# Kernel tuning notes

Hardware: AMD Instinct MI355X
Metric: run time of the kernel (lower is better)

Reference implementation:

```python
import jax, jax.numpy as jnp
import numpy as np

N_NODES = 100000
N_EDGES = 600000
D = 128


def setup_inputs() -> dict:
    key = jax.random.key(0)
    ks = jax.random.split(key, 12)
    inp = {
        'feat': jax.random.normal(ks[0], (N_NODES, D), dtype=jnp.float32),
        'W_tran': jax.random.normal(ks[1], (D, D), dtype=jnp.float32) * (1.0 / np.sqrt(D)),
        'att_w1': jax.random.normal(ks[2], (4 * D, D), dtype=jnp.float32) * (1.0 / np.sqrt(D)),
        'att_b1': jax.random.normal(ks[3], (4 * D,), dtype=jnp.float32) * 0.01,
        'att_w2': jax.random.normal(ks[4], (1, 4 * D), dtype=jnp.float32) * (1.0 / np.sqrt(4 * D)),
        'trans_w': jax.random.uniform(ks[5], (N_EDGES,), dtype=jnp.float32),
        'geo_src': jax.random.randint(ks[6], (N_EDGES,), 0, N_NODES, dtype=jnp.int32),
        'geo_dst': jax.random.randint(ks[7], (N_EDGES,), 0, N_NODES, dtype=jnp.int32),
        'cat_src': jax.random.randint(ks[8], (N_EDGES,), 0, N_NODES, dtype=jnp.int32),
        'cat_dst': jax.random.randint(ks[9], (N_EDGES,), 0, N_NODES, dtype=jnp.int32),
        'trans_src': jax.random.randint(ks[10], (N_EDGES,), 0, N_NODES, dtype=jnp.int32),
        'trans_dst': jax.random.randint(ks[11], (N_EDGES,), 0, N_NODES, dtype=jnp.int32),
    }
    return inp


def _mean_agg(f, src, dst, n):
    # copy_u('f','m') then mean('m', .) : gather src feats, segment-mean by dst
    msum = jax.ops.segment_sum(f[src], dst, num_segments=n)
    cnt = jax.ops.segment_sum(jnp.ones((src.shape[0],), f.dtype), dst, num_segments=n)
    return msum / jnp.maximum(cnt, 1.0)[:, None]


def reference(feat, W_tran, att_w1, att_b1, att_w2, trans_w,
              geo_src, geo_dst, cat_src, cat_dst, trans_src, trans_dst):
    n = feat.shape[0]
    # feat_tran: Linear(D, D, bias=False) -> x @ W^T
    f = feat @ W_tran.T
    geo = _mean_agg(f, geo_src, geo_dst, n)            # [N, D]
    cat = _mean_agg(f, cat_src, cat_dst, n)            # [N, D]
    # u_mul_e('f','w') then sum: weighted gather + segment-sum by dst
    trans = jax.ops.segment_sum(f[trans_src] * trans_w[:, None], trans_dst, num_segments=n)
    z = jnp.stack([geo, trans, cat], axis=1)           # [N, 3, D]
    # SemanticAttention: Linear -> tanh -> Linear(no bias), mean over nodes, softmax over relations
    h = jnp.tanh(jnp.einsum('nrd,hd->nrh', z, att_w1) + att_b1)   # [N, 3, 4D]
    w = jnp.einsum('nrh,oh->nro', h, att_w2).mean(0)              # [3, 1]
    beta = jax.nn.softmax(w, axis=0)                              # [3, 1]
    fused = (beta[None, :, :] * z).sum(1)                         # [N, D]
    return jax.nn.leaky_relu(fused, negative_slope=0.2)
```

## Files before the change

kernel.cpp:

```cpp
#include <hip/hip_runtime.h>
#include <math.h>

#define DD 128
#define NNODES 100000
#define NEDGES 600000
#define NREL 3
#define MTOT (NREL*NNODES)
#define NTILES (NNODES/16)
#define RT_PER_BLK 8
#define NBLK_REL ((NTILES + RT_PER_BLK - 1)/RT_PER_BLK)
#define ATT_WAVES 8

#define BSHIFT 10
#define NBUCK ((NNODES + 1023) >> BSHIFT)
#define GBUCK (NREL*NBUCK)
#define CAP 8192
#define P1_THREADS 512
#define P1_EPT 8
#define P1_EPB (P1_THREADS*P1_EPT)
#define P1_BLOCKS ((NREL*NEDGES + P1_EPB - 1)/P1_EPB)

typedef __attribute__((ext_vector_type(8))) short short8;
typedef __attribute__((ext_vector_type(4))) float f32x4;

__device__ inline float bf2f(unsigned short u){ return __uint_as_float(((unsigned int)u)<<16); }
__device__ inline float bflo(unsigned int u){ return __uint_as_float(u<<16); }
__device__ inline float bfhi(unsigned int u){ return __uint_as_float(u & 0xffff0000u); }
__device__ inline unsigned short f2bf(float f){
    unsigned int i = __float_as_uint(f);
    unsigned int r = (i + 0x7fffu + ((i>>16)&1u)) >> 16;
    return (unsigned short)r;
}
__device__ inline unsigned int pack2(float lo, float hi){
    return (unsigned int)f2bf(lo) | ((unsigned int)f2bf(hi) << 16);
}
__device__ inline short8 cvt8(const float* __restrict__ p){
    f32x4 a = *(const f32x4*)p;
    f32x4 b = *(const f32x4*)(p+4);
    short8 t;
    t[0]=(short)f2bf(a[0]); t[1]=(short)f2bf(a[1]); t[2]=(short)f2bf(a[2]); t[3]=(short)f2bf(a[3]);
    t[4]=(short)f2bf(b[0]); t[5]=(short)f2bf(b[1]); t[6]=(short)f2bf(b[2]); t[7]=(short)f2bf(b[3]);
    return t;
}

__global__ __launch_bounds__(256) void k_cvt2(
    const float* __restrict__ ina, unsigned short* __restrict__ outa, int na4,
    const float* __restrict__ inb, unsigned short* __restrict__ outb, int nb4)
{
    int gid = blockIdx.x*256 + threadIdx.x;
    const float* in; unsigned short* out; int idx;
    if (gid < na4){ in = ina; out = outa; idx = gid; }
    else { idx = gid - na4; if (idx >= nb4) return; in = inb; out = outb; }
    f32x4 v = ((const f32x4*)in)[idx];
    ushort4 o;
    o.x=f2bf(v[0]); o.y=f2bf(v[1]); o.z=f2bf(v[2]); o.w=f2bf(v[3]);
    ((ushort4*)out)[idx] = o;
}

__global__ __launch_bounds__(256) void k_transform(
    const float* __restrict__ feat, const unsigned short* __restrict__ Wbf,
    unsigned short* __restrict__ f_out)
{
    int wid = blockIdx.x*4 + (threadIdx.x>>6);
    if (wid >= NNODES/16) return;
    int lane = threadIdx.x & 63;
    int m = lane & 15, quad = lane >> 4;
    int n0 = wid*16;

    short8 a[4];
    const float* arow = feat + (size_t)(n0+m)*DD;
    #pragma unroll
    for (int ks=0; ks<4; ++ks) a[ks] = cvt8(arow + ks*32 + quad*8);

    #pragma unroll
    for (int ct=0; ct<8; ++ct){
        f32x4 acc = {0.f,0.f,0.f,0.f};
        const short8* brow = (const short8*)(Wbf + (size_t)(ct*16+m)*DD);
        #pragma unroll
        for (int ks=0; ks<4; ++ks){
            acc = __builtin_amdgcn_mfma_f32_16x16x32_bf16(a[ks], brow[ks*4+quad], acc, 0,0,0);
        }
        int col = ct*16 + m;
        #pragma unroll
        for (int i=0;i<4;++i)
            f_out[(size_t)(n0+quad*4+i)*DD + col] = f2bf(acc[i]);
    }
}

__global__ __launch_bounds__(P1_THREADS) void k_part(
    const int* __restrict__ s0, const int* __restrict__ d0,
    const int* __restrict__ s1, const int* __restrict__ d1,
    const int* __restrict__ s2, const int* __restrict__ d2,
    const float* __restrict__ tw,
    int* __restrict__ bcur,
    int2* __restrict__ slab, float* __restrict__ wslab)
{
    __shared__ int hist[GBUCK];
    for (int i=threadIdx.x; i<GBUCK; i+=P1_THREADS) hist[i]=0;
    __syncthreads();

    int e0 = blockIdx.x * P1_EPB;
    int ss[P1_EPT], dd_[P1_EPT], gb[P1_EPT]; float wv[P1_EPT];
    #pragma unroll
    for (int j=0;j<P1_EPT;++j){
        int e = e0 + j*P1_THREADS + threadIdx.x;
        gb[j] = -1;
        if (e < NREL*NEDGES){
            int rel = e / NEDGES; int i = e - rel*NEDGES;
            const int* s = (rel==0)?s0:(rel==1)?s1:s2;
            const int* d = (rel==0)?d0:(rel==1)?d1:d2;
            ss[j]=s[i]; dd_[j]=d[i];
            wv[j] = (rel==2)? tw[i] : 0.f;
            gb[j] = rel*NBUCK + (dd_[j]>>BSHIFT);
            atomicAdd(&hist[gb[j]], 1);
        }
    }
    __syncthreads();
    for (int i=threadIdx.x; i<GBUCK; i+=P1_THREADS){
        int c = hist[i];
        hist[i] = (c>0) ? atomicAdd(&bcur[i], c) : 0;
    }
    __syncthreads();
    #pragma unroll
    for (int j=0;j<P1_EPT;++j){
        if (gb[j] >= 0){
            int off = atomicAdd(&hist[gb[j]], 1);
            int2 pr; pr.x = ss[j]; pr.y = dd_[j];
            slab[(size_t)gb[j]*CAP + off] = pr;
            if (gb[j] >= 2*NBUCK) wslab[(size_t)(gb[j]-2*NBUCK)*CAP + off] = wv[j];
        }
    }
}

__global__ __launch_bounds__(512) void k_bscan(const int* __restrict__ bcur,
                                               int* __restrict__ bbase)
{
    __shared__ int sm[512];
    int t = threadIdx.x;
    sm[t] = (t<GBUCK)? bcur[t] : 0; __syncthreads();
    for (int off=1; off<512; off<<=1){
        int x = (t>=off)? sm[t-off] : 0;
        __syncthreads(); sm[t]+=x; __syncthreads();
    }
    if (t<GBUCK) bbase[t] = (t>0)? sm[t-1] : 0;
}

__global__ __launch_bounds__(512) void k_csr(
    const int2* __restrict__ slab, const float* __restrict__ wslab,
    const int* __restrict__ bcur, const int* __restrict__ bbase,
    int* __restrict__ offs, int* __restrict__ cnt,
    int* __restrict__ es, float* __restrict__ ewt)
{
    __shared__ int lcnt[1024];
    __shared__ int lsc[1024];
    __shared__ int psum[512];
    int gb = blockIdx.x;
    int rel = gb / NBUCK, b = gb - rel*NBUCK;
    int n0 = b << BSHIFT;
    int nn = min(1024, NNODES - n0);
    int ecount = bcur[gb];
    int base = bbase[gb];
    const int2* ep = slab + (size_t)gb*CAP;
    int t = threadIdx.x;

    lcnt[2*t] = 0; lcnt[2*t+1] = 0;
    __syncthreads();
    for (int i=t; i<ecount; i+=512)
        atomicAdd(&lcnt[ep[i].y - n0], 1);
    __syncthreads();
    int v0 = lcnt[2*t], v1 = lcnt[2*t+1];
    psum[t] = v0 + v1; __syncthreads();
    for (int off=1; off<512; off<<=1){
        int x = (t>=off)? psum[t-off] : 0;
        __syncthreads(); psum[t]+=x; __syncthreads();
    }
    int ex = (t>0)? psum[t-1] : 0;
    lsc[2*t] = ex; lsc[2*t+1] = ex + v0;
    __syncthreads();
    int relN = rel*NNODES;
    for (int i=t; i<nn; i+=512){
        offs[relN + n0 + i] = base + lsc[i];
        cnt [relN + n0 + i] = lcnt[i];
    }
    __syncthreads();
    for (int i=t; i<ecount; i+=512){
        int2 pr = ep[i];
        int pos = base + atomicAdd(&lsc[pr.y - n0], 1);
        es[pos] = pr.x;
        if (rel==2) ewt[pos - 2*NEDGES] = wslab[(size_t)b*CAP + i];
    }
}

__global__ __launch_bounds__(256) void k_agg(
    const unsigned short* __restrict__ f,
    const int* __restrict__ es, const float* __restrict__ ewt,
    const int* __restrict__ offs, const int* __restrict__ cnt,
    unsigned short* __restrict__ z)
{
    int gid = blockIdx.x*256 + threadIdx.x;
    int g = gid >> 4;
    if (g >= MTOT) return;
    int c = gid & 15;
    int rel = g / NNODES;
    int start = offs[g];
    int deg   = cnt[g];

    float a0=0,a1=0,a2=0,a3=0,a4=0,a5=0,a6=0,a7=0;
    int i = 0;
    for (; i+1 < deg; i += 2){
        int s0 = es[start+i], s1 = es[start+i+1];
        uint4 v0 = *(const uint4*)(f + (size_t)s0*DD + c*8);
        uint4 v1 = *(const uint4*)(f + (size_t)s1*DD + c*8);
        float w0 = (rel==2) ? ewt[start+i   - 2*NEDGES] : 1.f;
        float w1 = (rel==2) ? ewt[start+i+1 - 2*NEDGES] : 1.f;
        a0 += w0*bflo(v0.x); a1 += w0*bfhi(v0.x);
        a2 += w0*bflo(v0.y); a3 += w0*bfhi(v0.y);
        a4 += w0*bflo(v0.z); a5 += w0*bfhi(v0.z);
        a6 += w0*bflo(v0.w); a7 += w0*bfhi(v0.w);
        a0 += w1*bflo(v1.x); a1 += w1*bfhi(v1.x);
        a2 += w1*bflo(v1.y); a3 += w1*bfhi(v1.y);
        a4 += w1*bflo(v1.z); a5 += w1*bfhi(v1.z);
        a6 += w1*bflo(v1.w); a7 += w1*bfhi(v1.w);
    }
    if (i < deg){
        int s = es[start+i];
        float w = (rel==2) ? ewt[start+i - 2*NEDGES] : 1.f;
        uint4 v = *(const uint4*)(f + (size_t)s*DD + c*8);
        a0 += w*bflo(v.x); a1 += w*bfhi(v.x);
        a2 += w*bflo(v.y); a3 += w*bfhi(v.y);
        a4 += w*bflo(v.z); a5 += w*bfhi(v.z);
        a6 += w*bflo(v.w); a7 += w*bfhi(v.w);
    }
    float sc = (rel<2) ? 1.f/fmaxf((float)deg, 1.f) : 1.f;
    uint4 o;
    o.x = pack2(a0*sc, a1*sc);
    o.y = pack2(a2*sc, a3*sc);
    o.z = pack2(a4*sc, a5*sc);
    o.w = pack2(a6*sc, a7*sc);
    *(uint4*)(z + (size_t)g*DD + c*8) = o;
}

__global__ __launch_bounds__(512, 4) void k_att(
    const unsigned short* __restrict__ z,
    const unsigned short* __restrict__ w1,
    const float* __restrict__ bias1,
    const float* __restrict__ wv2,
    float* __restrict__ w_part)
{
    __shared__ uint4 sm[RT_PER_BLK*256];
    __shared__ float sred[ATT_WAVES];
    const float C2 = 2.8853900817779268f;

    int rel = blockIdx.x / NBLK_REL;
    int nb  = blockIdx.x % NBLK_REL;
    int trt0 = nb * RT_PER_BLK;
    int rt_count = min(RT_PER_BLK, NTILES - trt0);
    int row0 = trt0 * 16;
    const unsigned short* zrel = z + (size_t)rel*NNODES*DD;

    int lane = threadIdx.x & 63;
    int wv   = threadIdx.x >> 6;
    int m = lane & 15, quad = lane >> 4;

    short8 bq[16];
    float ww[4], bbc[4];
    #pragma unroll
    for (int ct=0; ct<4; ++ct){
        int col = (wv*4 + ct)*16 + m;
        const short8* brow = (const short8*)(w1 + (size_t)col*DD);
        #pragma unroll
        for (int ks=0; ks<4; ++ks) bq[ct*4+ks] = brow[ks*4 + quad];
        ww[ct]  = wv2[col];
        bbc[ct] = bias1[col] * C2;
    }

    int valid_rows = rt_count * 16;
    #pragma unroll
    for (int i=0; i<4; ++i){
        int u = i*512 + threadIdx.x;
        int row = u >> 4, kc = u & 15;
        if (row < valid_rows){
            uint4 v = *(const uint4*)(zrel + (size_t)(row0+row)*DD + kc*8);
            int rt = row >> 4, mm = row & 15;
            sm[rt*256 + kc*16 + (mm ^ kc)] = v;
        }
    }
    __syncthreads();

    const short8* smx = (const short8*)sm;
    float s_r[4] = {0.f,0.f,0.f,0.f};
    for (int rt=0; rt<rt_count; ++rt){
        int base = rt*256;
        short8 a0 = smx[base + (0  + quad)*16 + (m ^ (0  + quad))];
        short8 a1 = smx[base + (4  + quad)*16 + (m ^ (4  + quad))];
        short8 a2 = smx[base + (8  + quad)*16 + (m ^ (8  + quad))];
        short8 a3 = smx[base + (12 + quad)*16 + (m ^ (12 + quad))];
        #pragma unroll
        for (int ct=0; ct<4; ++ct){
            f32x4 acc = {0.f,0.f,0.f,0.f};
            acc = __builtin_amdgcn_mfma_f32_16x16x32_bf16(a0, bq[ct*4+0], acc, 0,0,0);
            acc = __builtin_amdgcn_mfma_f32_16x16x32_bf16(a1, bq[ct*4+1], acc, 0,0,0);
            acc = __builtin_amdgcn_mfma_f32_16x16x32_bf16(a2, bq[ct*4+2], acc, 0,0,0);
            acc = __builtin_amdgcn_mfma_f32_16x16x32_bf16(a3, bq[ct*4+3], acc, 0,0,0);
            #pragma unroll
            for (int i=0;i<4;++i){
                float e = __builtin_amdgcn_exp2f(__builtin_fmaf(acc[i], C2, bbc[ct]));
                s_r[ct] += __builtin_amdgcn_rcpf(e + 1.f);
            }
        }
    }
    float s_all = 0.f;
    #pragma unroll
    for (int ct=0; ct<4; ++ct)
        s_all += ww[ct]*(float)(4*rt_count) - 2.f*ww[ct]*s_r[ct];
    #pragma unroll
    for (int off=32; off; off>>=1) s_all += __shfl_xor(s_all, off);
    if (lane == 0) sred[wv] = s_all;
    __syncthreads();
    if (threadIdx.x == 0){
        float tt = 0.f;
        #pragma unroll
        for (int i=0;i<ATT_WAVES;++i) tt += sred[i];
        atomicAdd(&w_part[rel], tt);
    }
}

__global__ __launch_bounds__(256) void k_final(
    const unsigned short* __restrict__ z0, const unsigned short* __restrict__ z1,
    const unsigned short* __restrict__ z2,
    const float* __restrict__ w_part, float* __restrict__ out)
{
    int gid = blockIdx.x*256 + threadIdx.x;
    if (gid >= NNODES*DD/4) return;
    const float invN = 1.f / (float)NNODES;
    float w0 = w_part[0]*invN, w1 = w_part[1]*invN, w2 = w_part[2]*invN;
    float mx = fmaxf(w0, fmaxf(w1, w2));
    const float LOG2E = 1.4426950408889634f;
    float e0 = __builtin_amdgcn_exp2f((w0-mx)*LOG2E);
    float e1 = __builtin_amdgcn_exp2f((w1-mx)*LOG2E);
    float e2 = __builtin_amdgcn_exp2f((w2-mx)*LOG2E);
    float inv = 1.f/(e0+e1+e2);
    float b0 = e0*inv, b1 = e1*inv, b2 = e2*inv;
    ushort4 g = ((const ushort4*)z0)[gid];
    ushort4 t = ((const ushort4*)z1)[gid];
    ushort4 c = ((const ushort4*)z2)[gid];
    f32x4 o;
    float gv[4] = {bf2f(g.x),bf2f(g.y),bf2f(g.z),bf2f(g.w)};
    float tv[4] = {bf2f(t.x),bf2f(t.y),bf2f(t.z),bf2f(t.w)};
    float cv[4] = {bf2f(c.x),bf2f(c.y),bf2f(c.z),bf2f(c.w)};
    #pragma unroll
    for (int i=0;i<4;++i){
        float x = b0*gv[i] + b1*tv[i] + b2*cv[i];
        o[i] = (x > 0.f) ? x : 0.2f*x;
    }
    ((f32x4*)out)[gid] = o;
}

extern "C" void kernel_launch(void* const* d_in, const int* in_sizes, int n_in,
                              void* d_out, int out_size, void* d_ws, size_t ws_size,
                              hipStream_t stream)
{
    const float* feat = (const float*)d_in[0];
    const float* W    = (const float*)d_in[1];
    const float* aw1  = (const float*)d_in[2];
    const float* ab1  = (const float*)d_in[3];
    const float* aw2  = (const float*)d_in[4];
    const float* tw   = (const float*)d_in[5];
    const int* geo_src   = (const int*)d_in[6];
    const int* geo_dst   = (const int*)d_in[7];
    const int* cat_src   = (const int*)d_in[8];
    const int* cat_dst   = (const int*)d_in[9];
    const int* trans_src = (const int*)d_in[10];
    const int* trans_dst = (const int*)d_in[11];

    char* ws = (char*)d_ws;
    float* w_part = (float*)ws;
    int*   bcur   = (int*)(w_part + 64);
    int*   bbase  = bcur + 320;
    int*   offs   = bbase + 320;
    int*   cnt    = offs + MTOT;
    unsigned short* w1_bf = (unsigned short*)(cnt + MTOT);
    unsigned short* w_bf  = w1_bf + 512*DD;
    int*   es     = (int*)(w_bf + DD*DD);
    float* ewt    = (float*)(es + NREL*NEDGES);
    unsigned short* z = (unsigned short*)(ewt + NEDGES);
    int2*  slab   = (int2*)z;
    float* wslab  = (float*)(slab + (size_t)GBUCK*CAP);
    unsigned short* f_bf = (unsigned short*)d_out;

    (void)hipMemsetAsync(w_part, 0, (64 + 320)*sizeof(int), stream);

    int na4 = 512*DD/4, nb4 = DD*DD/4;
    k_cvt2<<<(na4 + nb4 + 255)/256, 256, 0, stream>>>(aw1, w1_bf, na4, W, w_bf, nb4);
    k_transform<<<(NNODES/16 + 3)/4, 256, 0, stream>>>(feat, w_bf, f_bf);

    k_part<<<P1_BLOCKS, P1_THREADS, 0, stream>>>(geo_src, geo_dst, cat_src, cat_dst,
                                                 trans_src, trans_dst, tw,
                                                 bcur, slab, wslab);
    k_bscan<<<1, 512, 0, stream>>>(bcur, bbase);
    k_csr<<<GBUCK, 512, 0, stream>>>(slab, wslab, bcur, bbase, offs, cnt, es, ewt);

    k_agg<<<(MTOT*16 + 255)/256, 256, 0, stream>>>(f_bf, es, ewt, offs, cnt, z);

    k_att<<<NREL*NBLK_REL, 512, 0, stream>>>(z, w1_bf, ab1, aw2, w_part);

    unsigned short* z_geo   = z;
    unsigned short* z_cat   = z + (size_t)NNODES*DD;
    unsigned short* z_trans = z + (size_t)2*NNODES*DD;
    int dg = (NNODES*DD/4 + 255)/256;
    k_final<<<dg, 256, 0, stream>>>(z_geo, z_cat, z_trans, w_part, (float*)d_out);
}
```

Measured before the change: 356.4 us.

## Fuse neighbor aggregation into attention kernel, writing tiles straight to LDS

Merges the separate aggregation kernel into the attention-score kernel. Each block aggregates its own 128 rows per relation and writes each result both to global z (still needed by the final kernel) and directly into the swizzled shared-memory tile. This removes one launch and the re-read of z from global memory before the MFMA stage. The trade-off is that the gather now runs under the attention kernel's launch bounds and occupancy. Each thread also handles four rows in sequence, which may limit latency hiding for the irregular gathers.

```diff
diff --git a/kernel.cpp b/kernel.cpp
--- a/kernel.cpp
+++ b/kernel.cpp
@@ -191,60 +191,14 @@
     }
 }
 
-__global__ __launch_bounds__(256) void k_agg(
+__global__ __launch_bounds__(512, 4) void k_aggatt(
     const unsigned short* __restrict__ f,
     const int* __restrict__ es, const float* __restrict__ ewt,
     const int* __restrict__ offs, const int* __restrict__ cnt,
-    unsigned short* __restrict__ z)
-{
-    int gid = blockIdx.x*256 + threadIdx.x;
-    int g = gid >> 4;
-    if (g >= MTOT) return;
-    int c = gid & 15;
-    int rel = g / NNODES;
-    int start = offs[g];
-    int deg   = cnt[g];
-
-    float a0=0,a1=0,a2=0,a3=0,a4=0,a5=0,a6=0,a7=0;
-    int i = 0;
-    for (; i+1 < deg; i += 2){
-        int s0 = es[start+i], s1 = es[start+i+1];
-        uint4 v0 = *(const uint4*)(f + (size_t)s0*DD + c*8);
-        uint4 v1 = *(const uint4*)(f + (size_t)s1*DD + c*8);
-        float w0 = (rel==2) ? ewt[start+i   - 2*NEDGES] : 1.f;
-        float w1 = (rel==2) ? ewt[start+i+1 - 2*NEDGES] : 1.f;
-        a0 += w0*bflo(v0.x); a1 += w0*bfhi(v0.x);
-        a2 += w0*bflo(v0.y); a3 += w0*bfhi(v0.y);
-        a4 += w0*bflo(v0.z); a5 += w0*bfhi(v0.z);
-        a6 += w0*bflo(v0.w); a7 += w0*bfhi(v0.w);
-        a0 += w1*bflo(v1.x); a1 += w1*bfhi(v1.x);
-        a2 += w1*bflo(v1.y); a3 += w1*bfhi(v1.y);
-        a4 += w1*bflo(v1.z); a5 += w1*bfhi(v1.z);
-        a6 += w1*bflo(v1.w); a7 += w1*bfhi(v1.w);
-    }
-    if (i < deg){
-        int s = es[start+i];
-        float w = (rel==2) ? ewt[start+i - 2*NEDGES] : 1.f;
-        uint4 v = *(const uint4*)(f + (size_t)s*DD + c*8);
-        a0 += w*bflo(v.x); a1 += w*bfhi(v.x);
-        a2 += w*bflo(v.y); a3 += w*bfhi(v.y);
-        a4 += w*bflo(v.z); a5 += w*bfhi(v.z);
-        a6 += w*bflo(v.w); a7 += w*bfhi(v.w);
-    }
-    float sc = (rel<2) ? 1.f/fmaxf((float)deg, 1.f) : 1.f;
-    uint4 o;
-    o.x = pack2(a0*sc, a1*sc);
-    o.y = pack2(a2*sc, a3*sc);
-    o.z = pack2(a4*sc, a5*sc);
-    o.w = pack2(a6*sc, a7*sc);
-    *(uint4*)(z + (size_t)g*DD + c*8) = o;
-}
-
-__global__ __launch_bounds__(512, 4) void k_att(
-    const unsigned short* __restrict__ z,
     const unsigned short* __restrict__ w1,
     const float* __restrict__ bias1,
     const float* __restrict__ wv2,
+    unsigned short* __restrict__ z,
     float* __restrict__ w_part)
 {
     __shared__ uint4 sm[RT_PER_BLK*256];
@@ -256,7 +210,56 @@
     int trt0 = nb * RT_PER_BLK;
     int rt_count = min(RT_PER_BLK, NTILES - trt0);
     int row0 = trt0 * 16;
-    const unsigned short* zrel = z + (size_t)rel*NNODES*DD;
+    int valid_rows = rt_count * 16;
+
+    int t = threadIdx.x;
+    int grp = t >> 4;
+    int c   = t & 15;
+    #pragma unroll
+    for (int pass=0; pass<4; ++pass){
+        int row = pass*32 + grp;
+        if (row < valid_rows){
+            int slot = rel*NNODES + row0 + row;
+            int start = offs[slot];
+            int deg   = cnt[slot];
+            float a0=0,a1=0,a2=0,a3=0,a4=0,a5=0,a6=0,a7=0;
+            int i = 0;
+            for (; i+1 < deg; i += 2){
+                int s0 = es[start+i], s1 = es[start+i+1];
+                uint4 v0 = *(const uint4*)(f + (size_t)s0*DD + c*8);
+                uint4 v1 = *(const uint4*)(f + (size_t)s1*DD + c*8);
+                float w0 = (rel==2) ? ewt[start+i   - 2*NEDGES] : 1.f;
+                float w1e = (rel==2) ? ewt[start+i+1 - 2*NEDGES] : 1.f;
+                a0 += w0*bflo(v0.x); a1 += w0*bfhi(v0.x);
+                a2 += w0*bflo(v0.y); a3 += w0*bfhi(v0.y);
+                a4 += w0*bflo(v0.z); a5 += w0*bfhi(v0.z);
+                a6 += w0*bflo(v0.w); a7 += w0*bfhi(v0.w);
+                a0 += w1e*bflo(v1.x); a1 += w1e*bfhi(v1.x);
+                a2 += w1e*bflo(v1.y); a3 += w1e*bfhi(v1.y);
+                a4 += w1e*bflo(v1.z); a5 += w1e*bfhi(v1.z);
+                a6 += w1e*bflo(v1.w); a7 += w1e*bfhi(v1.w);
+            }
+            if (i < deg){
+                int s = es[start+i];
+                float w = (rel==2) ? ewt[start+i - 2*NEDGES] : 1.f;
+                uint4 v = *(const uint4*)(f + (size_t)s*DD + c*8);
+                a0 += w*bflo(v.x); a1 += w*bfhi(v.x);
+                a2 += w*bflo(v.y); a3 += w*bfhi(v.y);
+                a4 += w*bflo(v.z); a5 += w*bfhi(v.z);
+                a6 += w*bflo(v.w); a7 += w*bfhi(v.w);
+            }
+            float sc = (rel<2) ? 1.f/fmaxf((float)deg, 1.f) : 1.f;
+            uint4 o;
+            o.x = pack2(a0*sc, a1*sc);
+            o.y = pack2(a2*sc, a3*sc);
+            o.z = pack2(a4*sc, a5*sc);
+            o.w = pack2(a6*sc, a7*sc);
+            *(uint4*)(z + (size_t)slot*DD + c*8) = o;
+            sm[(row>>4)*256 + c*16 + ((row&15) ^ c)] = o;
+        }
+    }
+    __syncthreads();
+    __builtin_amdgcn_sched_barrier(0);
 
     int lane = threadIdx.x & 63;
     int wv   = threadIdx.x >> 6;
@@ -273,19 +276,6 @@
         ww[ct]  = wv2[col];
         bbc[ct] = bias1[col] * C2;
     }
-
-    int valid_rows = rt_count * 16;
-    #pragma unroll
-    for (int i=0; i<4; ++i){
-        int u = i*512 + threadIdx.x;
-        int row = u >> 4, kc = u & 15;
-        if (row < valid_rows){
-            uint4 v = *(const uint4*)(zrel + (size_t)(row0+row)*DD + kc*8);
-            int rt = row >> 4, mm = row & 15;
-            sm[rt*256 + kc*16 + (mm ^ kc)] = v;
-        }
-    }
-    __syncthreads();
 
     const short8* smx = (const short8*)sm;
     float s_r[4] = {0.f,0.f,0.f,0.f};
@@ -400,9 +390,8 @@
     k_bscan<<<1, 512, 0, stream>>>(bcur, bbase);
     k_csr<<<GBUCK, 512, 0, stream>>>(slab, wslab, bcur, bbase, offs, cnt, es, ewt);
 
-    k_agg<<<(MTOT*16 + 255)/256, 256, 0, stream>>>(f_bf, es, ewt, offs, cnt, z);
-
-    k_att<<<NREL*NBLK_REL, 512, 0, stream>>>(z, w1_bf, ab1, aw2, w_part);
+    k_aggatt<<<NREL*NBLK_REL, 512, 0, stream>>>(f_bf, es, ewt, offs, cnt,
+                                                w1_bf, ab1, aw2, z, w_part);
 
     unsigned short* z_geo   = z;
     unsigned short* z_cat   = z + (size_t)NNODES*DD;
```

After: 372.6 us. 1.05x slower.
